# Kernel optimization log

Measured on AMD Instinct MI355X. Metric: run time of the kernel, lower is better.

## Reference

```python
import jax, jax.numpy as jnp
import numpy as np


def setup_inputs() -> dict:
    key = jax.random.key(0)
    k1, k2, k3, k4 = jax.random.split(key, 4)
    B, P, K = 512, 1024, 64  # batch, n_points, n_components
    x = jax.random.normal(k1, (B, P), dtype=jnp.float32)
    # params init: uniform(-0.01, 0.01) as in reset_parameters
    a = jax.random.uniform(k2, (P, K, 1), dtype=jnp.float32, minval=-0.01, maxval=0.01)
    b = jax.random.uniform(k3, (P, K, 1), dtype=jnp.float32, minval=-0.01, maxval=0.01)
    a0 = jax.random.uniform(k4, (1,), dtype=jnp.float32, minval=-0.01, maxval=0.01)
    return {"x": x, "a": a, "b": b, "a0": a0}


def reference(x, a, b, a0):
    # x: [B, P]; a, b: [P, K, 1]; a0: [1]
    P = x.shape[-1]
    K = a.shape[1]
    two_pi_over_P = jnp.asarray(2.0 * np.pi / P, dtype=x.dtype)
    n = jnp.arange(K, dtype=x.dtype)                    # component indices 0..K-1
    pa = x @ a[..., 0]                                  # [B, K]  (x @ a[:, n] batched)
    pb = x @ b[..., 0]                                  # [B, K]
    phase = two_pi_over_P * x[..., None] * n            # [B, P, K]
    out = (a0 / (2 * P)) * jnp.ones_like(x)             # a0/(2*n_points) * ones_like(x)
    out = out + jnp.einsum('bk,bpk->bp', pa, jnp.cos(phase))
    out = out + jnp.einsum('bk,bpk->bp', pb, jnp.sin(phase))
    return out
```

## Files before the change

### kernel.cpp

```cpp
#include <hip/hip_runtime.h>


constexpr int PN = 1024;
constexpr int KN = 64;
constexpr int ROWS = 2;

__global__ __launch_bounds__(256) void fourier_fused(
    const float* __restrict__ x,
    const float* __restrict__ a,
    const float* __restrict__ bco,
    const float* __restrict__ a0,
    float* __restrict__ out)
{
    __shared__ float xs[ROWS][PN];
    __shared__ float red[2][ROWS][16][KN];
    __shared__ float spab[ROWS][2 * KN];

    const int t = threadIdx.x;
    const int b0 = blockIdx.x * ROWS;

    #pragma unroll
    for (int r = 0; r < ROWS; ++r) {
        float4 v = ((const float4*)(x + (size_t)(b0 + r) * PN))[t];
        xs[r][4 * t + 0] = v.x;
        xs[r][4 * t + 1] = v.y;
        xs[r][4 * t + 2] = v.z;
        xs[r][4 * t + 3] = v.w;
    }
    __syncthreads();

    {
        const int kg = t & 15;
        const int pg = t >> 4;
        float sa[ROWS][4] = {};
        float sb[ROWS][4] = {};
        #pragma unroll 4
        for (int i = 0; i < 64; ++i) {
            const int p = pg + 16 * i;
            const float4 av = *(const float4*)(a   + p * KN + 4 * kg);
            const float4 bv = *(const float4*)(bco + p * KN + 4 * kg);
            #pragma unroll
            for (int r = 0; r < ROWS; ++r) {
                const float xv = xs[r][p];
                sa[r][0] = fmaf(xv, av.x, sa[r][0]);
                sa[r][1] = fmaf(xv, av.y, sa[r][1]);
                sa[r][2] = fmaf(xv, av.z, sa[r][2]);
                sa[r][3] = fmaf(xv, av.w, sa[r][3]);
                sb[r][0] = fmaf(xv, bv.x, sb[r][0]);
                sb[r][1] = fmaf(xv, bv.y, sb[r][1]);
                sb[r][2] = fmaf(xv, bv.z, sb[r][2]);
                sb[r][3] = fmaf(xv, bv.w, sb[r][3]);
            }
        }
        #pragma unroll
        for (int r = 0; r < ROWS; ++r) {
            #pragma unroll
            for (int j = 0; j < 4; ++j) {
                red[0][r][pg][4 * kg + j] = sa[r][j];
                red[1][r][pg][4 * kg + j] = sb[r][j];
            }
        }
    }
    __syncthreads();

    {
        const int which = t >> 7;
        const int r = (t >> 6) & (ROWS - 1);
        const int k = t & 63;
        float s = 0.f;
        #pragma unroll
        for (int pg = 0; pg < 16; ++pg) s += red[which][r][pg][k];
        spab[r][2 * k + which] = s;
    }
    __syncthreads();

    const float c0 = a0[0] * (1.0f / (2.0f * (float)PN));
    const float tp = (float)(6.283185307179586 / (double)PN);

    #pragma unroll
    for (int r = 0; r < ROWS; ++r) {
        float cm1[4], sm1[4], cm2[4], sm2[4], t2[4], acc[4];
        const float pa0 = spab[r][0];
        const float pa1 = spab[r][2];
        const float pb1 = spab[r][3];
        #pragma unroll
        for (int j = 0; j < 4; ++j) {
            const float th = tp * xs[r][4 * t + j];
            float c1, s1;
            __sincosf(th, &s1, &c1);
            t2[j]  = c1 + c1;
            cm2[j] = 1.f; sm2[j] = 0.f;
            cm1[j] = c1;  sm1[j] = s1;
            acc[j] = fmaf(pa1, c1, fmaf(pb1, s1, c0 + pa0));
        }
        #pragma unroll 8
        for (int k = 2; k < KN; ++k) {
            const float2 pk = *(const float2*)&spab[r][2 * k];
            #pragma unroll
            for (int j = 0; j < 4; ++j) {
                const float ck = fmaf(t2[j], cm1[j], -cm2[j]);
                const float sk = fmaf(t2[j], sm1[j], -sm2[j]);
                acc[j] = fmaf(pk.x, ck, acc[j]);
                acc[j] = fmaf(pk.y, sk, acc[j]);
                cm2[j] = cm1[j]; cm1[j] = ck;
                sm2[j] = sm1[j]; sm1[j] = sk;
            }
        }
        float4 o;
        o.x = acc[0]; o.y = acc[1]; o.z = acc[2]; o.w = acc[3];
        ((float4*)(out + (size_t)(b0 + r) * PN))[t] = o;
    }
}

extern "C" void kernel_launch(void* const* d_in, const int* in_sizes, int n_in,
                              void* d_out, int out_size, void* d_ws, size_t ws_size,
                              hipStream_t stream) {
    const float* x  = (const float*)d_in[0];
    const float* a  = (const float*)d_in[1];
    const float* b  = (const float*)d_in[2];
    const float* a0 = (const float*)d_in[3];
    float* out = (float*)d_out;

    const int nblocks = (out_size / PN) / ROWS;
    fourier_fused<<<dim3(nblocks), dim3(256), 0, stream>>>(x, a, b, a0, out);
}
```

Baseline: 72.06 us.

## Split into tiled partial-GEMM kernel and separate Chebyshev output kernel

Replaces the single fused kernel, which re-read all of a and b (256KB each) for every pair of batch rows, with two kernels. The first tiles the projection over batch and point chunks, so each block reads only a 64-point slice of a and b for 32 batch rows, and writes partial sums to workspace. The second reduces the 16 partials per row and evaluates the Chebyshev cos/sin recurrence, one row per block. This cuts redundant coefficient traffic, at the cost of a second launch and a workspace round trip of about 4MB written and read back.

```diff
diff --git a/kernel.cpp b/kernel.cpp
--- a/kernel.cpp
+++ b/kernel.cpp
@@ -3,113 +3,120 @@
 
 constexpr int PN = 1024;
 constexpr int KN = 64;
-constexpr int ROWS = 2;
 
-__global__ __launch_bounds__(256) void fourier_fused(
+__global__ __launch_bounds__(256) void k_partial(
     const float* __restrict__ x,
     const float* __restrict__ a,
     const float* __restrict__ bco,
-    const float* __restrict__ a0,
-    float* __restrict__ out)
+    float* __restrict__ pw)
 {
-    __shared__ float xs[ROWS][PN];
-    __shared__ float red[2][ROWS][16][KN];
-    __shared__ float spab[ROWS][2 * KN];
+    __shared__ float xs[32][64];
 
     const int t = threadIdx.x;
-    const int b0 = blockIdx.x * ROWS;
-
-    #pragma unroll
-    for (int r = 0; r < ROWS; ++r) {
-        float4 v = ((const float4*)(x + (size_t)(b0 + r) * PN))[t];
-        xs[r][4 * t + 0] = v.x;
-        xs[r][4 * t + 1] = v.y;
-        xs[r][4 * t + 2] = v.z;
-        xs[r][4 * t + 3] = v.w;
-    }
-    __syncthreads();
+    const int pc = blockIdx.x;
+    const int bt = blockIdx.y;
+    const int p0 = pc * 64;
+    const int b0 = bt * 32;
 
     {
-        const int kg = t & 15;
-        const int pg = t >> 4;
-        float sa[ROWS][4] = {};
-        float sb[ROWS][4] = {};
-        #pragma unroll 4
-        for (int i = 0; i < 64; ++i) {
-            const int p = pg + 16 * i;
-            const float4 av = *(const float4*)(a   + p * KN + 4 * kg);
-            const float4 bv = *(const float4*)(bco + p * KN + 4 * kg);
-            #pragma unroll
-            for (int r = 0; r < ROWS; ++r) {
-                const float xv = xs[r][p];
-                sa[r][0] = fmaf(xv, av.x, sa[r][0]);
-                sa[r][1] = fmaf(xv, av.y, sa[r][1]);
-                sa[r][2] = fmaf(xv, av.z, sa[r][2]);
-                sa[r][3] = fmaf(xv, av.w, sa[r][3]);
-                sb[r][0] = fmaf(xv, bv.x, sb[r][0]);
-                sb[r][1] = fmaf(xv, bv.y, sb[r][1]);
-                sb[r][2] = fmaf(xv, bv.z, sb[r][2]);
-                sb[r][3] = fmaf(xv, bv.w, sb[r][3]);
-            }
-        }
+        const int c = t & 15, row = t >> 4;
         #pragma unroll
-        for (int r = 0; r < ROWS; ++r) {
-            #pragma unroll
-            for (int j = 0; j < 4; ++j) {
-                red[0][r][pg][4 * kg + j] = sa[r][j];
-                red[1][r][pg][4 * kg + j] = sb[r][j];
-            }
+        for (int h = 0; h < 2; ++h) {
+            const int r = row + 16 * h;
+            const float4 v = *(const float4*)(x + (size_t)(b0 + r) * PN + p0 + 4 * c);
+            xs[r][4 * c + 0] = v.x; xs[r][4 * c + 1] = v.y;
+            xs[r][4 * c + 2] = v.z; xs[r][4 * c + 3] = v.w;
         }
     }
     __syncthreads();
 
-    {
-        const int which = t >> 7;
-        const int r = (t >> 6) & (ROWS - 1);
-        const int k = t & 63;
+    const int kg = t & 15;
+    const int bg = t >> 4;
+    float sa[2][4] = {{0.f}}, sb[2][4] = {{0.f}};
+    #pragma unroll 4
+    for (int i = 0; i < 64; ++i) {
+        const int p = p0 + i;
+        const float4 av = *(const float4*)(a   + (size_t)p * KN + 4 * kg);
+        const float4 bv = *(const float4*)(bco + (size_t)p * KN + 4 * kg);
+        #pragma unroll
+        for (int r = 0; r < 2; ++r) {
+            const float xv = xs[2 * bg + r][i];
+            sa[r][0] = fmaf(xv, av.x, sa[r][0]);
+            sa[r][1] = fmaf(xv, av.y, sa[r][1]);
+            sa[r][2] = fmaf(xv, av.z, sa[r][2]);
+            sa[r][3] = fmaf(xv, av.w, sa[r][3]);
+            sb[r][0] = fmaf(xv, bv.x, sb[r][0]);
+            sb[r][1] = fmaf(xv, bv.y, sb[r][1]);
+            sb[r][2] = fmaf(xv, bv.z, sb[r][2]);
+            sb[r][3] = fmaf(xv, bv.w, sb[r][3]);
+        }
+    }
+
+    #pragma unroll
+    for (int r = 0; r < 2; ++r) {
+        float* dst = pw + (((size_t)(b0 + 2 * bg + r) * 16 + pc) * 128) + 8 * kg;
+        #pragma unroll
+        for (int j = 0; j < 4; ++j) {
+            float2 v; v.x = sa[r][j]; v.y = sb[r][j];
+            *(float2*)(dst + 2 * j) = v;
+        }
+    }
+}
+
+__global__ __launch_bounds__(256) void k_out(
+    const float* __restrict__ x,
+    const float* __restrict__ pw,
+    const float* __restrict__ a0,
+    float* __restrict__ out)
+{
+    __shared__ float spab[2 * KN];
+
+    const int t = threadIdx.x;
+    const int b = blockIdx.x;
+
+    if (t < 128) {
+        const float* src = pw + (size_t)b * (16 * 128) + t;
         float s = 0.f;
         #pragma unroll
-        for (int pg = 0; pg < 16; ++pg) s += red[which][r][pg][k];
-        spab[r][2 * k + which] = s;
+        for (int pc = 0; pc < 16; ++pc) s += src[pc * 128];
+        spab[t] = s;
     }
     __syncthreads();
 
+    const float4 xv4 = ((const float4*)(x + (size_t)b * PN))[t];
+    const float xv[4] = {xv4.x, xv4.y, xv4.z, xv4.w};
     const float c0 = a0[0] * (1.0f / (2.0f * (float)PN));
     const float tp = (float)(6.283185307179586 / (double)PN);
 
+    float cm1[4], sm1[4], cm2[4], sm2[4], t2[4], acc[4];
+    const float pa0 = spab[0];
+    const float pa1 = spab[2];
+    const float pb1 = spab[3];
     #pragma unroll
-    for (int r = 0; r < ROWS; ++r) {
-        float cm1[4], sm1[4], cm2[4], sm2[4], t2[4], acc[4];
-        const float pa0 = spab[r][0];
-        const float pa1 = spab[r][2];
-        const float pb1 = spab[r][3];
+    for (int j = 0; j < 4; ++j) {
+        const float th = tp * xv[j];
+        float c1, s1;
+        __sincosf(th, &s1, &c1);
+        t2[j]  = c1 + c1;
+        cm2[j] = 1.f; sm2[j] = 0.f;
+        cm1[j] = c1;  sm1[j] = s1;
+        acc[j] = fmaf(pa1, c1, fmaf(pb1, s1, c0 + pa0));
+    }
+    #pragma unroll 8
+    for (int k = 2; k < KN; ++k) {
+        const float2 pk = *(const float2*)&spab[2 * k];
         #pragma unroll
         for (int j = 0; j < 4; ++j) {
-            const float th = tp * xs[r][4 * t + j];
-            float c1, s1;
-            __sincosf(th, &s1, &c1);
-            t2[j]  = c1 + c1;
-            cm2[j] = 1.f; sm2[j] = 0.f;
-            cm1[j] = c1;  sm1[j] = s1;
-            acc[j] = fmaf(pa1, c1, fmaf(pb1, s1, c0 + pa0));
+            const float ck = fmaf(t2[j], cm1[j], -cm2[j]);
+            const float sk = fmaf(t2[j], sm1[j], -sm2[j]);
+            acc[j] = fmaf(pk.x, ck, acc[j]);
+            acc[j] = fmaf(pk.y, sk, acc[j]);
+            cm2[j] = cm1[j]; cm1[j] = ck;
+            sm2[j] = sm1[j]; sm1[j] = sk;
         }
-        #pragma unroll 8
-        for (int k = 2; k < KN; ++k) {
-            const float2 pk = *(const float2*)&spab[r][2 * k];
-            #pragma unroll
-            for (int j = 0; j < 4; ++j) {
-                const float ck = fmaf(t2[j], cm1[j], -cm2[j]);
-                const float sk = fmaf(t2[j], sm1[j], -sm2[j]);
-                acc[j] = fmaf(pk.x, ck, acc[j]);
-                acc[j] = fmaf(pk.y, sk, acc[j]);
-                cm2[j] = cm1[j]; cm1[j] = ck;
-                sm2[j] = sm1[j]; sm1[j] = sk;
-            }
-        }
-        float4 o;
-        o.x = acc[0]; o.y = acc[1]; o.z = acc[2]; o.w = acc[3];
-        ((float4*)(out + (size_t)(b0 + r) * PN))[t] = o;
     }
+    float4 o; o.x = acc[0]; o.y = acc[1]; o.z = acc[2]; o.w = acc[3];
+    ((float4*)(out + (size_t)b * PN))[t] = o;
 }
 
 extern "C" void kernel_launch(void* const* d_in, const int* in_sizes, int n_in,
@@ -120,7 +127,8 @@
     const float* b  = (const float*)d_in[2];
     const float* a0 = (const float*)d_in[3];
     float* out = (float*)d_out;
+    float* pw  = (float*)d_ws;
 
-    const int nblocks = (out_size / PN) / ROWS;
-    fourier_fused<<<dim3(nblocks), dim3(256), 0, stream>>>(x, a, b, a0, out);
+    k_partial<<<dim3(16, 16), dim3(256), 0, stream>>>(x, a, b, pw);
+    k_out<<<dim3(512), dim3(256), 0, stream>>>(x, pw, a0, out);
 }
```

After: 84.57 us. 1.17x slower.

## Split projection into two K halves and overlap the second with the Chebyshev recurrence

Applied to the files above, without the earlier changes.

The x@a and x@b projection is now done in two halves of 32 components. The load and FMA of the second half are interleaved with the cos/sin recurrence that consumes the first half's coefficients. The recurrence and the projection use packed v_pk_fma_f32/v_pk_mul_f32 on (cos, sin) pairs, and the reduction buffer is padded. This is meant to hide global-load latency behind ALU work and roughly halve the VALU instruction count, at the cost of more registers, an extra reduction pass with barriers, and a hardcoded grid of 256 blocks.

```diff
diff --git a/kernel.cpp b/kernel.cpp
--- a/kernel.cpp
+++ b/kernel.cpp
@@ -1,9 +1,21 @@
 #include <hip/hip_runtime.h>
 
 
+typedef float f2 __attribute__((ext_vector_type(2)));
+
+__device__ __forceinline__ f2 pk_fma(f2 a, f2 b, f2 c) {
+    f2 d;
+    asm("v_pk_fma_f32 %0, %1, %2, %3" : "=v"(d) : "v"(a), "v"(b), "v"(c));
+    return d;
+}
+__device__ __forceinline__ f2 pk_mul(f2 a, f2 b) {
+    f2 d;
+    asm("v_pk_mul_f32 %0, %1, %2" : "=v"(d) : "v"(a), "v"(b));
+    return d;
+}
+
 constexpr int PN = 1024;
 constexpr int KN = 64;
-constexpr int ROWS = 2;
 
 __global__ __launch_bounds__(256) void fourier_fused(
     const float* __restrict__ x,
@@ -12,102 +24,155 @@
     const float* __restrict__ a0,
     float* __restrict__ out)
 {
-    __shared__ float xs[ROWS][PN];
-    __shared__ float red[2][ROWS][16][KN];
-    __shared__ float spab[ROWS][2 * KN];
+    __shared__ float xs[2][PN];
+    __shared__ float red[2][2][32][34];
+    __shared__ float spab[2][64];
 
     const int t = threadIdx.x;
-    const int b0 = blockIdx.x * ROWS;
+    const int b0 = 2 * blockIdx.x;
 
     #pragma unroll
-    for (int r = 0; r < ROWS; ++r) {
-        float4 v = ((const float4*)(x + (size_t)(b0 + r) * PN))[t];
-        xs[r][4 * t + 0] = v.x;
-        xs[r][4 * t + 1] = v.y;
-        xs[r][4 * t + 2] = v.z;
-        xs[r][4 * t + 3] = v.w;
+    for (int r = 0; r < 2; ++r)
+        *(float4*)&xs[r][4 * t] = ((const float4*)(x + (size_t)(b0 + r) * PN))[t];
+    __syncthreads();
+
+    const int kg = t & 7;
+    const int pg = t >> 3;
+
+    f2 sa01[2] = {}, sa23[2] = {}, sb01[2] = {}, sb23[2] = {};
+    #pragma unroll 2
+    for (int i = 0; i < 32; ++i) {
+        const int p = pg + 32 * i;
+        const float4 av = *(const float4*)(a   + (size_t)p * KN + 4 * kg);
+        const float4 bv = *(const float4*)(bco + (size_t)p * KN + 4 * kg);
+        #pragma unroll
+        for (int r = 0; r < 2; ++r) {
+            const float xv = xs[r][p];
+            const f2 xx = {xv, xv};
+            sa01[r] = pk_fma(xx, f2{av.x, av.y}, sa01[r]);
+            sa23[r] = pk_fma(xx, f2{av.z, av.w}, sa23[r]);
+            sb01[r] = pk_fma(xx, f2{bv.x, bv.y}, sb01[r]);
+            sb23[r] = pk_fma(xx, f2{bv.z, bv.w}, sb23[r]);
+        }
+    }
+    #pragma unroll
+    for (int r = 0; r < 2; ++r) {
+        *(f2*)&red[0][r][pg][4 * kg]     = sa01[r];
+        *(f2*)&red[0][r][pg][4 * kg + 2] = sa23[r];
+        *(f2*)&red[1][r][pg][4 * kg]     = sb01[r];
+        *(f2*)&red[1][r][pg][4 * kg + 2] = sb23[r];
+    }
+    __syncthreads();
+    if (t < 128) {
+        const int ab = (t >> 6) & 1, r = (t >> 5) & 1, k = t & 31;
+        float s = 0.f;
+        #pragma unroll
+        for (int g = 0; g < 32; ++g) s += red[ab][r][g][k];
+        spab[r][2 * k + ab] = s;
     }
     __syncthreads();
 
-    {
-        const int kg = t & 15;
-        const int pg = t >> 4;
-        float sa[ROWS][4] = {};
-        float sb[ROWS][4] = {};
-        #pragma unroll 4
-        for (int i = 0; i < 64; ++i) {
-            const int p = pg + 16 * i;
-            const float4 av = *(const float4*)(a   + p * KN + 4 * kg);
-            const float4 bv = *(const float4*)(bco + p * KN + 4 * kg);
-            #pragma unroll
-            for (int r = 0; r < ROWS; ++r) {
-                const float xv = xs[r][p];
-                sa[r][0] = fmaf(xv, av.x, sa[r][0]);
-                sa[r][1] = fmaf(xv, av.y, sa[r][1]);
-                sa[r][2] = fmaf(xv, av.z, sa[r][2]);
-                sa[r][3] = fmaf(xv, av.w, sa[r][3]);
-                sb[r][0] = fmaf(xv, bv.x, sb[r][0]);
-                sb[r][1] = fmaf(xv, bv.y, sb[r][1]);
-                sb[r][2] = fmaf(xv, bv.z, sb[r][2]);
-                sb[r][3] = fmaf(xv, bv.w, sb[r][3]);
-            }
-        }
-        #pragma unroll
-        for (int r = 0; r < ROWS; ++r) {
-            #pragma unroll
-            for (int j = 0; j < 4; ++j) {
-                red[0][r][pg][4 * kg + j] = sa[r][j];
-                red[1][r][pg][4 * kg + j] = sb[r][j];
-            }
-        }
-    }
-    __syncthreads();
+    const float c0b = a0[0] * (1.0f / (2.0f * (float)PN));
+    const float tp  = (float)(6.283185307179586 / (double)PN);
+    const f2 negone = {-1.f, -1.f};
 
-    {
-        const int which = t >> 7;
-        const int r = (t >> 6) & (ROWS - 1);
-        const int k = t & 63;
-        float s = 0.f;
-        #pragma unroll
-        for (int pg = 0; pg < 16; ++pg) s += red[which][r][pg][k];
-        spab[r][2 * k + which] = s;
-    }
-    __syncthreads();
-
-    const float c0 = a0[0] * (1.0f / (2.0f * (float)PN));
-    const float tp = (float)(6.283185307179586 / (double)PN);
-
+    f2 p1[2][4], np2[2][4], acc[2][4], t2v[2][4];
     #pragma unroll
-    for (int r = 0; r < ROWS; ++r) {
-        float cm1[4], sm1[4], cm2[4], sm2[4], t2[4], acc[4];
+    for (int r = 0; r < 2; ++r) {
         const float pa0 = spab[r][0];
-        const float pa1 = spab[r][2];
-        const float pb1 = spab[r][3];
         #pragma unroll
         for (int j = 0; j < 4; ++j) {
             const float th = tp * xs[r][4 * t + j];
             float c1, s1;
             __sincosf(th, &s1, &c1);
-            t2[j]  = c1 + c1;
-            cm2[j] = 1.f; sm2[j] = 0.f;
-            cm1[j] = c1;  sm1[j] = s1;
-            acc[j] = fmaf(pa1, c1, fmaf(pb1, s1, c0 + pa0));
+            p1[r][j]  = f2{c1, s1};
+            np2[r][j] = f2{-1.f, 0.f};
+            t2v[r][j] = f2{c1 + c1, c1 + c1};
+            acc[r][j] = f2{c0b + pa0, 0.f};
         }
-        #pragma unroll 8
-        for (int k = 2; k < KN; ++k) {
-            const float2 pk = *(const float2*)&spab[r][2 * k];
+    }
+
+    f2 ta01[2] = {}, ta23[2] = {}, tb01[2] = {}, tb23[2] = {};
+    {
+        const int p = pg;
+        const float4 av = *(const float4*)(a   + (size_t)p * KN + 32 + 4 * kg);
+        const float4 bv = *(const float4*)(bco + (size_t)p * KN + 32 + 4 * kg);
+        #pragma unroll
+        for (int r = 0; r < 2; ++r) {
+            const float xv = xs[r][p];
+            const f2 xx = {xv, xv};
+            ta01[r] = pk_fma(xx, f2{av.x, av.y}, ta01[r]);
+            ta23[r] = pk_fma(xx, f2{av.z, av.w}, ta23[r]);
+            tb01[r] = pk_fma(xx, f2{bv.x, bv.y}, tb01[r]);
+            tb23[r] = pk_fma(xx, f2{bv.z, bv.w}, tb23[r]);
+        }
+    }
+    #pragma unroll 2
+    for (int i = 1; i < 32; ++i) {
+        const int p = pg + 32 * i;
+        const float4 av = *(const float4*)(a   + (size_t)p * KN + 32 + 4 * kg);
+        const float4 bv = *(const float4*)(bco + (size_t)p * KN + 32 + 4 * kg);
+        #pragma unroll
+        for (int r = 0; r < 2; ++r) {
+            const f2 coef = *(const f2*)&spab[r][2 * i];
             #pragma unroll
             for (int j = 0; j < 4; ++j) {
-                const float ck = fmaf(t2[j], cm1[j], -cm2[j]);
-                const float sk = fmaf(t2[j], sm1[j], -sm2[j]);
-                acc[j] = fmaf(pk.x, ck, acc[j]);
-                acc[j] = fmaf(pk.y, sk, acc[j]);
-                cm2[j] = cm1[j]; cm1[j] = ck;
-                sm2[j] = sm1[j]; sm1[j] = sk;
+                acc[r][j] = pk_fma(coef, p1[r][j], acc[r][j]);
+                const f2 pn = pk_fma(t2v[r][j], p1[r][j], np2[r][j]);
+                np2[r][j] = pk_mul(p1[r][j], negone);
+                p1[r][j]  = pn;
             }
         }
+        #pragma unroll
+        for (int r = 0; r < 2; ++r) {
+            const float xv = xs[r][p];
+            const f2 xx = {xv, xv};
+            ta01[r] = pk_fma(xx, f2{av.x, av.y}, ta01[r]);
+            ta23[r] = pk_fma(xx, f2{av.z, av.w}, ta23[r]);
+            tb01[r] = pk_fma(xx, f2{bv.x, bv.y}, tb01[r]);
+            tb23[r] = pk_fma(xx, f2{bv.z, bv.w}, tb23[r]);
+        }
+    }
+    __syncthreads();
+    #pragma unroll
+    for (int r = 0; r < 2; ++r) {
+        *(f2*)&red[0][r][pg][4 * kg]     = ta01[r];
+        *(f2*)&red[0][r][pg][4 * kg + 2] = ta23[r];
+        *(f2*)&red[1][r][pg][4 * kg]     = tb01[r];
+        *(f2*)&red[1][r][pg][4 * kg + 2] = tb23[r];
+    }
+    __syncthreads();
+    if (t < 128) {
+        const int ab = (t >> 6) & 1, r = (t >> 5) & 1, k = t & 31;
+        float s = 0.f;
+        #pragma unroll
+        for (int g = 0; g < 32; ++g) s += red[ab][r][g][k];
+        spab[r][2 * k + ab] = s;
+    }
+    __syncthreads();
+
+    #pragma unroll 4
+    for (int kk = 0; kk < 32; ++kk) {
+        #pragma unroll
+        for (int r = 0; r < 2; ++r) {
+            const f2 coef = *(const f2*)&spab[r][2 * kk];
+            #pragma unroll
+            for (int j = 0; j < 4; ++j) {
+                acc[r][j] = pk_fma(coef, p1[r][j], acc[r][j]);
+                const f2 pn = pk_fma(t2v[r][j], p1[r][j], np2[r][j]);
+                np2[r][j] = pk_mul(p1[r][j], negone);
+                p1[r][j]  = pn;
+            }
+        }
+    }
+
+    #pragma unroll
+    for (int r = 0; r < 2; ++r) {
         float4 o;
-        o.x = acc[0]; o.y = acc[1]; o.z = acc[2]; o.w = acc[3];
+        o.x = acc[r][0].x + acc[r][0].y;
+        o.y = acc[r][1].x + acc[r][1].y;
+        o.z = acc[r][2].x + acc[r][2].y;
+        o.w = acc[r][3].x + acc[r][3].y;
         ((float4*)(out + (size_t)(b0 + r) * PN))[t] = o;
     }
 }
@@ -121,6 +186,5 @@
     const float* a0 = (const float*)d_in[3];
     float* out = (float*)d_out;
 
-    const int nblocks = (out_size / PN) / ROWS;
-    fourier_fused<<<dim3(nblocks), dim3(256), 0, stream>>>(x, a, b, a0, out);
+    fourier_fused<<<dim3(256), dim3(256), 0, stream>>>(x, a, b, a0, out);
 }
```

New measurement: 77.72 us. 7.9% more time.
